# Kernel tuning notes

Hardware: AMD Instinct MI355X
Metric: run time of the kernel (lower is better)

Reference implementation:

```python
import jax, jax.numpy as jnp
import numpy as np

EPS = 1e-8
TINY = 1e-12
C_L1 = float(np.sqrt(3.0 / (4.0 * np.pi)))  # integral-normalized l=1 SH coefficient


def _elu_feature_map(x):
    # positive_feature_map(kind='elu'): elu(x) + 1 > 0
    return jax.nn.elu(x) + 1.0


def _sph_bessel_j1(x):
    # j1(x) = sin(x)/x^2 - cos(x)/x, with series x/3 near 0 for stability
    small = x < 1e-4
    xs = jnp.where(small, 1.0, x)
    return jnp.where(small, x / 3.0, jnp.sin(xs) / (xs * xs) - jnp.cos(xs) / xs)


def setup_inputs() -> dict:
    key = jax.random.key(0)
    k1, k2, k3, k4, k5 = jax.random.split(key, 5)
    B, N, H, D, C, Q = 1, 2048, 8, 32, 32, 8
    pos = jax.random.normal(k1, (B, N, 3), dtype=jnp.float32) * 5.0
    q = jax.random.normal(k2, (B, N, H, D), dtype=jnp.float32)
    k = jax.random.normal(k3, (B, N, H, D), dtype=jnp.float32)
    v = jax.random.normal(k4, (B, N, H, C), dtype=jnp.float32)
    kappa = jnp.linspace(0.5, 4.0, Q, dtype=jnp.float32)          # (Q,) buffer
    a = jax.random.normal(k5, (H, Q), dtype=jnp.float32) * 0.1    # (H,Q) -> 'head' mode
    node_mask = jnp.ones((B, N), dtype=bool)
    return {"pos": pos, "q": q, "k": k, "v": v, "kappa": kappa, "a": a, "node_mask": node_mask}


def reference(pos, q, k, v, kappa, a, node_mask):
    B, N = pos.shape[0], pos.shape[1]
    m = node_mask.astype(pos.dtype)  # (B,N)

    # Linear (kernel) attention: alpha[b,h,i,j] = <phi(q_i), phi(k_j)> / sum_n <phi(q_i), phi(k_n)>
    phi_q = _elu_feature_map(q) * m[:, :, None, None]
    phi_k = _elu_feature_map(k) * m[:, :, None, None]
    v_m = v * m[:, :, None, None]
    logits = jnp.einsum('bihd,bjhd->bhij', phi_q, phi_k)
    denom = jnp.maximum(logits.sum(axis=-1, keepdims=True), EPS)
    alpha = logits / denom  # (B,H,N,N)

    # Pairwise geometry
    r_ij = pos[:, :, None, :] - pos[:, None, :, :]            # (B,N,N,3)
    dist = jnp.sqrt(jnp.sum(r_ij * r_ij, axis=-1) + TINY)     # (B,N,N)
    eye = jnp.eye(N, dtype=bool)
    safe_vec = jnp.array([1.0, 0.0, 0.0], dtype=pos.dtype)
    r_safe = jnp.where(eye[None, :, :, None], safe_vec, r_ij)

    # Real spherical harmonics, l=1, integral normalization, on normalized r_ij
    rn = jnp.sqrt(jnp.sum(r_safe * r_safe, axis=-1, keepdims=True) + TINY)
    Y = C_L1 * (r_safe / rn)  # (B,N,N,3) -> M=3 components

    # Radial part: f[b,h,i,j] = sum_q a[h,q] * j1(dist_ij * kappa_q)
    x = dist[..., None] * kappa  # (B,N,N,Q)
    jl = _sph_bessel_j1(x)
    f = jnp.einsum('bijq,hq->bhij', jl, a)

    # out[b,i,h,m,c] = sum_j alpha*f * Y * v
    w = alpha * f
    out = jnp.einsum('bhij,bijm,bjhc->bihmc', w, Y, v_m)
    return out  # (B, N, H, 2l+1=3, C)
```

## Files before the change

### kernel.cpp

```cpp
#include <hip/hip_runtime.h>

#define NN   2048
#define NH   8
#define ND   32
#define NC   32
#define NQ   8
#define JS   8
#define NOUT (NN*NH*3*NC)
#define EPSV 1e-8f
#define TINYV 1e-12f
#define C_L1 0.4886025119029199f
#define PSCALE 128.0f

typedef _Float16 half8 __attribute__((ext_vector_type(8)));
typedef __fp16   fp16x2 __attribute__((ext_vector_type(2)));
typedef float    f32x4 __attribute__((ext_vector_type(4)));
typedef float    f32x2 __attribute__((ext_vector_type(2)));

__device__ __forceinline__ float phi_elu(float x) { return x > 0.f ? x + 1.f : __expf(x); }
__device__ __forceinline__ float rfl(float x) {
    return __int_as_float(__builtin_amdgcn_readfirstlane(__float_as_int(x)));
}
__device__ __forceinline__ void glds16(const void* g, void* l) {
    __builtin_amdgcn_global_load_lds(
        (const __attribute__((address_space(1))) void*)g,
        (__attribute__((address_space(3))) void*)l, 16, 0, 0);
}

__global__ void k_prep(const float* __restrict__ pos, const float* __restrict__ q,
                       const float* __restrict__ k, const float* __restrict__ v,
                       const float* __restrict__ kappa, const float* __restrict__ a,
                       _Float16* __restrict__ phiQ16, _Float16* __restrict__ KtF,
                       _Float16* __restrict__ VtF, float* __restrict__ posT,
                       float* __restrict__ ksum, float* __restrict__ coef) {
    int b = blockIdx.x, t = threadIdx.x;
    if (b < 256) {
        int h = t >> 5, d = t & 31;
        int dg = d >> 3, e = d & 7;
        float ks = 0.f;
        for (int jj = 0; jj < 8; ++jj) {
            int j = b * 8 + jj;
            float pq = phi_elu(q[j * 256 + t]);
            float pk = phi_elu(k[j * 256 + t]);
            phiQ16[j * 256 + t] = (_Float16)pq;
            int jblk = j >> 5, jin = j & 31, jf = jin >> 4, lo = jin & 15;
            KtF[((((h * 64 + jblk) * 2 + jf) * 64) + dg * 16 + lo) * 8 + e] = (_Float16)pk;
            ks += pk;
        }
        atomicAdd(&ksum[t], ks);
    } else if (b < 512) {
        int unit = (b - 256) * 4 + (t >> 6);
        int lane = t & 63;
        int h = unit >> 7, jblk = (unit >> 1) & 63, cf = unit & 1;
        int hgrp = h >> 1, hh = h & 1;
        int c = cf * 16 + (lane & 15);
        int g8 = lane >> 4;
        half8 w0, w1, w2, w3;
        #pragma unroll
        for (int e = 0; e < 8; ++e) {
            int jl = g8 * 4 + (e & 3) + 16 * (e >> 2);
            int j = jblk * 32 + jl;
            float vv = v[(j * NH + h) * NC + c];
            w0[e] = (_Float16)vv;
            w1[e] = (_Float16)(vv * pos[j * 3 + 0]);
            w2[e] = (_Float16)(vv * pos[j * 3 + 1]);
            w3[e] = (_Float16)(vv * pos[j * 3 + 2]);
        }
        size_t fb = ((size_t)(jblk * 4 + hgrp) * 16 + hh * 2 + cf) * 64 + lane;
        ((half8*)VtF)[fb]        = w0;
        ((half8*)VtF)[fb + 256]  = w1;
        ((half8*)VtF)[fb + 512]  = w2;
        ((half8*)VtF)[fb + 768]  = w3;
    } else if (b < 536) {
        int idx = (b - 512) * 256 + t;
        if (idx < 3 * NN) {
            int comp = idx >> 11, j = idx & 2047;
            posT[comp * NN + j] = pos[j * 3 + comp];
        }
    } else {
        if (t < NH) {
            float An[8];
            #pragma unroll
            for (int n = 0; n < 8; ++n) An[n] = a[t * NQ + n];
            float k0 = kappa[0];
            float ik0 = 1.f / k0, ik02 = ik0 * ik0;
            const float Tc[9][9] = {
                {0,0,0,0,0,0,0,0,0},
                {0,1,0,0,0,0,0,0,0},
                {-1,0,2,0,0,0,0,0,0},
                {0,-3,0,4,0,0,0,0,0},
                {1,0,-8,0,8,0,0,0,0},
                {0,5,0,-20,0,16,0,0,0},
                {-1,0,18,0,-48,0,32,0,0},
                {0,-7,0,56,0,-112,0,64,0},
                {1,0,-32,0,160,0,-256,0,128}};
            const float Uc[9][8] = {
                {0,0,0,0,0,0,0,0},
                {1,0,0,0,0,0,0,0},
                {0,2,0,0,0,0,0,0},
                {-1,0,4,0,0,0,0,0},
                {0,-4,0,8,0,0,0,0},
                {1,0,-12,0,16,0,0,0},
                {0,6,0,-32,0,32,0,0},
                {-1,0,24,0,-80,0,64,0},
                {0,-8,0,80,0,-192,0,128}};
            #pragma unroll
            for (int kk = 0; kk < 9; ++kk) {
                float s = 0.f;
                #pragma unroll
                for (int n = 1; n <= 8; ++n) s = fmaf(An[n-1] * (1.f / n), Tc[n][kk], s);
                coef[kk * 8 + t] = s * ik0;
            }
            #pragma unroll
            for (int kk = 0; kk < 8; ++kk) {
                float s = 0.f;
                #pragma unroll
                for (int n = 1; n <= 8; ++n) s = fmaf(An[n-1] * (1.f / (n * n)), Uc[n][kk], s);
                coef[(9 + kk) * 8 + t] = s * ik02;
            }
        }
    }
}

__global__ __launch_bounds__(256, 3)
void k_main(const float* __restrict__ posT, const _Float16* __restrict__ phiQ16,
            const _Float16* __restrict__ KtF, const _Float16* __restrict__ VtF,
            const float* __restrict__ kappa, const float* __restrict__ coef,
            const float* __restrict__ ksum, _Float16* __restrict__ part) {
    __shared__ __align__(16) char smem[2 * 16384];
    int tid = threadIdx.x;
    int wid = tid >> 6, lane = tid & 63;
    int li = lane & 15, g = lane >> 4;

    int bid = blockIdx.x;
    int hgrp = bid & 3, js = (bid >> 2) & 7, ib = bid >> 5;
    int itile = ib * 64 + wid * 16;

    float k0 = rfl(kappa[0]);

    float pc0[2];
    f32x2 cpq[2][8];
    #pragma unroll
    for (int hh = 0; hh < 2; ++hh) {
        int h = hgrp * 2 + hh;
        pc0[hh] = rfl(coef[h]);
        cpq[hh][0][0] = rfl(coef[8 * 8 + h]);
        cpq[hh][0][1] = rfl(coef[(9 + 7) * 8 + h]);
        #pragma unroll
        for (int kk = 1; kk <= 7; ++kk) {
            cpq[hh][kk][0] = rfl(coef[kk * 8 + h]);
            cpq[hh][kk][1] = rfl(coef[(9 + kk - 1) * 8 + h]);
        }
    }

    half8 qa[2];
    #pragma unroll
    for (int hh = 0; hh < 2; ++hh)
        qa[hh] = ((const half8*)phiQ16)[((size_t)(itile + li) * NH + hgrp * 2 + hh) * 4 + g];

    float pi0 = posT[itile + li];
    float pi1 = posT[NN + itile + li];
    float pi2 = posT[2 * NN + itile + li];

    f32x4 acc[2][4][2];
    #pragma unroll
    for (int hh = 0; hh < 2; ++hh)
      #pragma unroll
      for (int pl = 0; pl < 4; ++pl)
        #pragma unroll
        for (int cf = 0; cf < 2; ++cf)
          acc[hh][pl][cf] = (f32x4){0.f, 0.f, 0.f, 0.f};

    const int j0 = js * (NN / JS);
    const int NCHUNK = (NN / JS) / 32;
    const f32x4 z4 = (f32x4){0.f, 0.f, 0.f, 0.f};
    const int soff = wid * 4096 + lane * 16;

    half8 kf[2][2], kfn[2][2];
    {
        int jblk0 = j0 >> 5;
        #pragma unroll
        for (int hh = 0; hh < 2; ++hh)
            #pragma unroll
            for (int jF = 0; jF < 2; ++jF)
                kf[hh][jF] = ((const half8*)KtF)[
                    (((hgrp * 2 + hh) * 64 + jblk0) * 2 + jF) * 64 + lane];
        size_t sl = (size_t)(jblk0 * 4 + hgrp);
        const char* src = (const char*)VtF + (sl << 14) + soff;
        char* dstl = smem + soff;
        #pragma unroll
        for (int kk = 0; kk < 4; ++kk)
            glds16(src + kk * 1024, dstl + kk * 1024);
    }

    #pragma unroll 1
    for (int t = 0; t < NCHUNK; ++t) {
        int jc = j0 + t * 32, jblk = jc >> 5;

        union { half8 h; fp16x2 p[4]; } wa[2];

        #pragma unroll
        for (int jF = 0; jF < 2; ++jF) {
            f32x4 pj4[3];
            #pragma unroll
            for (int m = 0; m < 3; ++m)
                pj4[m] = *(const f32x4*)(posT + m * NN + jc + jF * 16 + g * 4);

            f32x4 s[2];
            #pragma unroll
            for (int hh = 0; hh < 2; ++hh)
                s[hh] = __builtin_amdgcn_mfma_f32_16x16x32_f16(kf[hh][jF], qa[hh], z4, 0, 0, 0);

            float gux[2][4];
            #pragma unroll
            for (int r = 0; r < 4; ++r) {
                float dx = pi0 - pj4[0][r];
                float dy = pi1 - pj4[1][r];
                float dz = pi2 - pj4[2][r];
                float d2 = fmaf(dx, dx, fmaf(dy, dy, fmaf(dz, dz, TINYV)));
                float u = rsqrtf(d2);
                u = (d2 < 1e-10f) ? 0.f : u;
                float dist = d2 * u;
                float th = dist * k0;
                float sth, cth;
                __sincosf(th, &sth, &cth);
                float e1 = u * u;
                float ws = u * sth;
                f32x2 cc; cc[0] = cth; cc[1] = cth;
                #pragma unroll
                for (int hh = 0; hh < 2; ++hh) {
                    f32x2 pq = cpq[hh][0];
                    #pragma unroll
                    for (int kk = 7; kk >= 1; --kk)
                        pq = __builtin_elementwise_fma(pq, cc, cpq[hh][kk]);
                    float P = fmaf(pq[0], cth, pc0[hh]);
                    float inner = fmaf(ws, pq[1], -P);
                    gux[hh][r] = (s[hh][r] * e1) * inner;
                }
            }
            #pragma unroll
            for (int hh = 0; hh < 2; ++hh) {
                wa[hh].p[jF * 2 + 0] = __builtin_amdgcn_cvt_pkrtz(gux[hh][0], gux[hh][1]);
                wa[hh].p[jF * 2 + 1] = __builtin_amdgcn_cvt_pkrtz(gux[hh][2], gux[hh][3]);
            }
        }

        __syncthreads();

        if (t + 1 < NCHUNK) {
            int jn = jblk + 1;
            #pragma unroll
            for (int hh = 0; hh < 2; ++hh)
                #pragma unroll
                for (int jF = 0; jF < 2; ++jF)
                    kfn[hh][jF] = ((const half8*)KtF)[
                        (((hgrp * 2 + hh) * 64 + jn) * 2 + jF) * 64 + lane];
            size_t sl = (size_t)(jn * 4 + hgrp);
            const char* src = (const char*)VtF + (sl << 14) + soff;
            char* dstl = smem + ((t + 1) & 1) * 16384 + soff;
            #pragma unroll
            for (int kk = 0; kk < 4; ++kk)
                glds16(src + kk * 1024, dstl + kk * 1024);
        }

        const char* vb = smem + (t & 1) * 16384;
        #pragma unroll
        for (int hh = 0; hh < 2; ++hh) {
            #pragma unroll
            for (int pl = 0; pl < 4; ++pl) {
                half8 vf0 = *(const half8*)(vb + ((pl * 4 + hh * 2 + 0) * 1024) + lane * 16);
                half8 vf1 = *(const half8*)(vb + ((pl * 4 + hh * 2 + 1) * 1024) + lane * 16);
                acc[hh][pl][0] = __builtin_amdgcn_mfma_f32_16x16x32_f16(wa[hh].h, vf0, acc[hh][pl][0], 0, 0, 0);
                acc[hh][pl][1] = __builtin_amdgcn_mfma_f32_16x16x32_f16(wa[hh].h, vf1, acc[hh][pl][1], 0, 0, 0);
            }
        }

        if (t + 1 < NCHUNK) {
            #pragma unroll
            for (int hh = 0; hh < 2; ++hh)
                #pragma unroll
                for (int jF = 0; jF < 2; ++jF)
                    kf[hh][jF] = kfn[hh][jF];
        }
    }

    f32x4 pi_ep[3];
    #pragma unroll
    for (int m = 0; m < 3; ++m)
        pi_ep[m] = *(const f32x4*)(posT + m * NN + itile + g * 4);

    float dinvC[2][4];
    #pragma unroll
    for (int hh = 0; hh < 2; ++hh) {
        int h = hgrp * 2 + hh;
        float p = 0.f;
        #pragma unroll
        for (int e = 0; e < 8; ++e) p += (float)qa[hh][e] * ksum[h * 32 + g * 8 + e];
        p += __shfl_xor(p, 16);
        p += __shfl_xor(p, 32);
        float dcol = (C_L1 * PSCALE) / fmaxf(p, EPSV);
        #pragma unroll
        for (int r = 0; r < 4; ++r)
            dinvC[hh][r] = __shfl(dcol, g * 4 + r);
    }

    _Float16* pdst = part + (size_t)js * NOUT;
    #pragma unroll
    for (int hh = 0; hh < 2; ++hh) {
        int h = hgrp * 2 + hh;
        #pragma unroll
        for (int m = 0; m < 3; ++m)
        #pragma unroll
        for (int cf = 0; cf < 2; ++cf)
        #pragma unroll
        for (int r = 0; r < 4; ++r) {
            int i = itile + g * 4 + r;
            size_t idx = ((size_t)i * NH + h) * 96 + m * 32 + cf * 16 + li;
            float val = fmaf(pi_ep[m][r], acc[hh][0][cf][r], -acc[hh][m + 1][cf][r]);
            pdst[idx] = (_Float16)(val * dinvC[hh][r]);
        }
    }
}

__global__ void k_reduce(const _Float16* __restrict__ part, float4* __restrict__ out) {
    int e = blockIdx.x * 256 + threadIdx.x;
    const int NO8 = NOUT / 8;
    if (e >= NO8) return;
    float s[8] = {0.f, 0.f, 0.f, 0.f, 0.f, 0.f, 0.f, 0.f};
    #pragma unroll
    for (int p = 0; p < JS; ++p) {
        half8 t = ((const half8*)part)[(size_t)p * NO8 + e];
        #pragma unroll
        for (int x = 0; x < 8; ++x) s[x] += (float)t[x];
    }
    const float S = 1.f / PSCALE;
    out[e * 2]     = make_float4(s[0] * S, s[1] * S, s[2] * S, s[3] * S);
    out[e * 2 + 1] = make_float4(s[4] * S, s[5] * S, s[6] * S, s[7] * S);
}

extern "C" void kernel_launch(void* const* d_in, const int* in_sizes, int n_in,
                              void* d_out, int out_size, void* d_ws, size_t ws_size,
                              hipStream_t stream) {
    const float* pos   = (const float*)d_in[0];
    const float* q     = (const float*)d_in[1];
    const float* k     = (const float*)d_in[2];
    const float* v     = (const float*)d_in[3];
    const float* kappa = (const float*)d_in[4];
    const float* a     = (const float*)d_in[5];
    float* out = (float*)d_out;
    char* ws = (char*)d_ws;

    _Float16* phiQ16 = (_Float16*)(ws + 0);
    _Float16* KtF    = (_Float16*)(ws + (1u << 20));
    _Float16* VtF    = (_Float16*)(ws + (2u << 20));
    float*    posT   = (float*)   (ws + (6u << 20));
    float*    ksum   = (float*)   (ws + (6u << 20) + 24576);
    float*    coefb  = (float*)   (ws + (6u << 20) + 91136);
    _Float16* partb  = (_Float16*)(ws + (6u << 20) + 131072);

    (void)hipMemsetAsync(ksum, 0, 256 * sizeof(float), stream);
    k_prep<<<537, 256, 0, stream>>>(pos, q, k, v, kappa, a,
                                    phiQ16, KtF, VtF, posT, ksum, coefb);
    k_main<<<(NN / 64) * 4 * JS, 256, 0, stream>>>(posT, phiQ16, KtF, VtF,
                                                   kappa, coefb, ksum, partb);
    k_reduce<<<(NOUT / 8 + 255) / 256, 256, 0, stream>>>(partb, (float4*)out);
}
```

Measured before the change: 68.74 us.

## Stage K and V layout transforms through LDS in prep and drop K register prefetch

The prep kernel now handles whole 32-row blocks per workgroup. It stages phi(k) and v/pos in shared memory, so the transposed KtF and VtF writes become coalesced 16-byte stores instead of scattered halfword writes, and it issues far fewer ksum atomics. The coefficient computation moves into its own tiny kernel, which adds one more launch. In the main kernel, the K fragments are now loaded directly inside the loop instead of being prefetched into registers, and the V LDS prefetch is issued after the MFMA block. This lowers register pressure but exposes K load latency and shortens the window in which the V prefetch can overlap.

```diff
diff --git a/kernel.cpp b/kernel.cpp
--- a/kernel.cpp
+++ b/kernel.cpp
@@ -27,98 +27,113 @@
         (__attribute__((address_space(3))) void*)l, 16, 0, 0);
 }
 
-__global__ void k_prep(const float* __restrict__ pos, const float* __restrict__ q,
-                       const float* __restrict__ k, const float* __restrict__ v,
-                       const float* __restrict__ kappa, const float* __restrict__ a,
-                       _Float16* __restrict__ phiQ16, _Float16* __restrict__ KtF,
-                       _Float16* __restrict__ VtF, float* __restrict__ posT,
-                       float* __restrict__ ksum, float* __restrict__ coef) {
+__global__ __launch_bounds__(256)
+void k_prep(const float* __restrict__ pos, const float* __restrict__ q,
+            const float* __restrict__ k, const float* __restrict__ v,
+            _Float16* __restrict__ phiQ16, _Float16* __restrict__ KtF,
+            _Float16* __restrict__ VtF, float* __restrict__ posT,
+            float* __restrict__ ksum) {
+    __shared__ __align__(16) char smem[33280];
     int b = blockIdx.x, t = threadIdx.x;
-    if (b < 256) {
-        int h = t >> 5, d = t & 31;
-        int dg = d >> 3, e = d & 7;
-        float ks = 0.f;
-        for (int jj = 0; jj < 8; ++jj) {
-            int j = b * 8 + jj;
+    int wid = t >> 6, lane = t & 63;
+    if (b < 64) {
+        _Float16* lds_k = (_Float16*)smem;
+        int jblk = b;
+        #pragma unroll 4
+        for (int jj = 0; jj < 32; ++jj) {
+            int j = jblk * 32 + jj;
             float pq = phi_elu(q[j * 256 + t]);
             float pk = phi_elu(k[j * 256 + t]);
             phiQ16[j * 256 + t] = (_Float16)pq;
-            int jblk = j >> 5, jin = j & 31, jf = jin >> 4, lo = jin & 15;
-            KtF[((((h * 64 + jblk) * 2 + jf) * 64) + dg * 16 + lo) * 8 + e] = (_Float16)pk;
-            ks += pk;
-        }
-        atomicAdd(&ksum[t], ks);
-    } else if (b < 512) {
-        int unit = (b - 256) * 4 + (t >> 6);
-        int lane = t & 63;
-        int h = unit >> 7, jblk = (unit >> 1) & 63, cf = unit & 1;
-        int hgrp = h >> 1, hh = h & 1;
-        int c = cf * 16 + (lane & 15);
-        int g8 = lane >> 4;
-        half8 w0, w1, w2, w3;
-        #pragma unroll
-        for (int e = 0; e < 8; ++e) {
-            int jl = g8 * 4 + (e & 3) + 16 * (e >> 2);
-            int j = jblk * 32 + jl;
-            float vv = v[(j * NH + h) * NC + c];
-            w0[e] = (_Float16)vv;
-            w1[e] = (_Float16)(vv * pos[j * 3 + 0]);
-            w2[e] = (_Float16)(vv * pos[j * 3 + 1]);
-            w3[e] = (_Float16)(vv * pos[j * 3 + 2]);
-        }
-        size_t fb = ((size_t)(jblk * 4 + hgrp) * 16 + hh * 2 + cf) * 64 + lane;
-        ((half8*)VtF)[fb]        = w0;
-        ((half8*)VtF)[fb + 256]  = w1;
-        ((half8*)VtF)[fb + 512]  = w2;
-        ((half8*)VtF)[fb + 768]  = w3;
-    } else if (b < 536) {
-        int idx = (b - 512) * 256 + t;
-        if (idx < 3 * NN) {
-            int comp = idx >> 11, j = idx & 2047;
-            posT[comp * NN + j] = pos[j * 3 + comp];
+            lds_k[jj * 264 + t] = (_Float16)pk;
+        }
+        __syncthreads();
+        float s = 0.f;
+        #pragma unroll
+        for (int jj = 0; jj < 32; ++jj) s += (float)lds_k[jj * 264 + t];
+        atomicAdd(&ksum[t], s);
+        int lo = lane & 15, dg = lane >> 4;
+        #pragma unroll
+        for (int uu = 0; uu < 4; ++uu) {
+            int unit = wid * 4 + uu;
+            int h = unit >> 1, jf = unit & 1;
+            half8 kf = *(const half8*)&lds_k[(jf * 16 + lo) * 264 + h * 32 + dg * 8];
+            ((half8*)KtF)[(size_t)((h * 64 + jblk) * 2 + jf) * 64 + lane] = kf;
         }
     } else {
-        if (t < NH) {
-            float An[8];
-            #pragma unroll
-            for (int n = 0; n < 8; ++n) An[n] = a[t * NQ + n];
-            float k0 = kappa[0];
-            float ik0 = 1.f / k0, ik02 = ik0 * ik0;
-            const float Tc[9][9] = {
-                {0,0,0,0,0,0,0,0,0},
-                {0,1,0,0,0,0,0,0,0},
-                {-1,0,2,0,0,0,0,0,0},
-                {0,-3,0,4,0,0,0,0,0},
-                {1,0,-8,0,8,0,0,0,0},
-                {0,5,0,-20,0,16,0,0,0},
-                {-1,0,18,0,-48,0,32,0,0},
-                {0,-7,0,56,0,-112,0,64,0},
-                {1,0,-32,0,160,0,-256,0,128}};
-            const float Uc[9][8] = {
-                {0,0,0,0,0,0,0,0},
-                {1,0,0,0,0,0,0,0},
-                {0,2,0,0,0,0,0,0},
-                {-1,0,4,0,0,0,0,0},
-                {0,-4,0,8,0,0,0,0},
-                {1,0,-12,0,16,0,0,0},
-                {0,6,0,-32,0,32,0,0},
-                {-1,0,24,0,-80,0,64,0},
-                {0,-8,0,80,0,-192,0,128}};
-            #pragma unroll
-            for (int kk = 0; kk < 9; ++kk) {
-                float s = 0.f;
-                #pragma unroll
-                for (int n = 1; n <= 8; ++n) s = fmaf(An[n-1] * (1.f / n), Tc[n][kk], s);
-                coef[kk * 8 + t] = s * ik0;
-            }
-            #pragma unroll
-            for (int kk = 0; kk < 8; ++kk) {
-                float s = 0.f;
-                #pragma unroll
-                for (int n = 1; n <= 8; ++n) s = fmaf(An[n-1] * (1.f / (n * n)), Uc[n][kk], s);
-                coef[(9 + kk) * 8 + t] = s * ik02;
-            }
-        }
+        float* lds_v = (float*)smem;
+        float* lds_p = (float*)(smem + 32768);
+        int jblk = b - 64;
+        #pragma unroll 4
+        for (int jj = 0; jj < 32; ++jj)
+            lds_v[jj * 256 + t] = v[(size_t)(jblk * 32 + jj) * 256 + t];
+        if (t < 96) lds_p[t] = pos[jblk * 96 + t];
+        __syncthreads();
+        if (t < 96) {
+            int m = t >> 5, jj = t & 31;
+            posT[m * NN + jblk * 32 + jj] = lds_p[jj * 3 + m];
+        }
+        int li = lane & 15, g8 = lane >> 4;
+        #pragma unroll
+        for (int uu = 0; uu < 16; ++uu) {
+            int unit = wid * 16 + uu;
+            int hgrp = unit >> 4, pl = (unit >> 2) & 3, hh = (unit >> 1) & 1, cf = unit & 1;
+            int h = hgrp * 2 + hh, c = cf * 16 + li;
+            half8 w;
+            #pragma unroll
+            for (int e = 0; e < 8; ++e) {
+                int jl = g8 * 4 + (e & 3) + 16 * (e >> 2);
+                float vv = lds_v[jl * 256 + h * 32 + c];
+                float fac = (pl == 0) ? 1.f : lds_p[jl * 3 + (pl - 1)];
+                w[e] = (_Float16)(vv * fac);
+            }
+            ((half8*)VtF)[((size_t)(jblk * 4 + hgrp) * 16 + pl * 4 + hh * 2 + cf) * 64 + lane] = w;
+        }
+    }
+}
+
+__global__ void k_coef(const float* __restrict__ kappa, const float* __restrict__ a,
+                       float* __restrict__ coef) {
+    int t = threadIdx.x;
+    if (t >= NH) return;
+    float An[8];
+    #pragma unroll
+    for (int n = 0; n < 8; ++n) An[n] = a[t * NQ + n];
+    float k0 = kappa[0];
+    float ik0 = 1.f / k0, ik02 = ik0 * ik0;
+    const float Tc[9][9] = {
+        {0,0,0,0,0,0,0,0,0},
+        {0,1,0,0,0,0,0,0,0},
+        {-1,0,2,0,0,0,0,0,0},
+        {0,-3,0,4,0,0,0,0,0},
+        {1,0,-8,0,8,0,0,0,0},
+        {0,5,0,-20,0,16,0,0,0},
+        {-1,0,18,0,-48,0,32,0,0},
+        {0,-7,0,56,0,-112,0,64,0},
+        {1,0,-32,0,160,0,-256,0,128}};
+    const float Uc[9][8] = {
+        {0,0,0,0,0,0,0,0},
+        {1,0,0,0,0,0,0,0},
+        {0,2,0,0,0,0,0,0},
+        {-1,0,4,0,0,0,0,0},
+        {0,-4,0,8,0,0,0,0},
+        {1,0,-12,0,16,0,0,0},
+        {0,6,0,-32,0,32,0,0},
+        {-1,0,24,0,-80,0,64,0},
+        {0,-8,0,80,0,-192,0,128}};
+    #pragma unroll
+    for (int kk = 0; kk < 9; ++kk) {
+        float s = 0.f;
+        #pragma unroll
+        for (int n = 1; n <= 8; ++n) s = fmaf(An[n-1] * (1.f / n), Tc[n][kk], s);
+        coef[kk * 8 + t] = s * ik0;
+    }
+    #pragma unroll
+    for (int kk = 0; kk < 8; ++kk) {
+        float s = 0.f;
+        #pragma unroll
+        for (int n = 1; n <= 8; ++n) s = fmaf(An[n-1] * (1.f / (n * n)), Uc[n][kk], s);
+        coef[(9 + kk) * 8 + t] = s * ik02;
     }
 }
 
@@ -176,16 +191,8 @@
     const f32x4 z4 = (f32x4){0.f, 0.f, 0.f, 0.f};
     const int soff = wid * 4096 + lane * 16;
 
-    half8 kf[2][2], kfn[2][2];
     {
-        int jblk0 = j0 >> 5;
-        #pragma unroll
-        for (int hh = 0; hh < 2; ++hh)
-            #pragma unroll
-            for (int jF = 0; jF < 2; ++jF)
-                kf[hh][jF] = ((const half8*)KtF)[
-                    (((hgrp * 2 + hh) * 64 + jblk0) * 2 + jF) * 64 + lane];
-        size_t sl = (size_t)(jblk0 * 4 + hgrp);
+        size_t sl = (size_t)((j0 >> 5) * 4 + hgrp);
         const char* src = (const char*)VtF + (sl << 14) + soff;
         char* dstl = smem + soff;
         #pragma unroll
@@ -208,8 +215,11 @@
 
             f32x4 s[2];
             #pragma unroll
-            for (int hh = 0; hh < 2; ++hh)
-                s[hh] = __builtin_amdgcn_mfma_f32_16x16x32_f16(kf[hh][jF], qa[hh], z4, 0, 0, 0);
+            for (int hh = 0; hh < 2; ++hh) {
+                int h = hgrp * 2 + hh;
+                half8 kf = ((const half8*)KtF)[(size_t)((h * 64 + jblk) * 2 + jF) * 64 + lane];
+                s[hh] = __builtin_amdgcn_mfma_f32_16x16x32_f16(kf, qa[hh], z4, 0, 0, 0);
+            }
 
             float gux[2][4];
             #pragma unroll
@@ -247,22 +257,6 @@
 
         __syncthreads();
 
-        if (t + 1 < NCHUNK) {
-            int jn = jblk + 1;
-            #pragma unroll
-            for (int hh = 0; hh < 2; ++hh)
-                #pragma unroll
-                for (int jF = 0; jF < 2; ++jF)
-                    kfn[hh][jF] = ((const half8*)KtF)[
-                        (((hgrp * 2 + hh) * 64 + jn) * 2 + jF) * 64 + lane];
-            size_t sl = (size_t)(jn * 4 + hgrp);
-            const char* src = (const char*)VtF + (sl << 14) + soff;
-            char* dstl = smem + ((t + 1) & 1) * 16384 + soff;
-            #pragma unroll
-            for (int kk = 0; kk < 4; ++kk)
-                glds16(src + kk * 1024, dstl + kk * 1024);
-        }
-
         const char* vb = smem + (t & 1) * 16384;
         #pragma unroll
         for (int hh = 0; hh < 2; ++hh) {
@@ -276,11 +270,12 @@
         }
 
         if (t + 1 < NCHUNK) {
-            #pragma unroll
-            for (int hh = 0; hh < 2; ++hh)
-                #pragma unroll
-                for (int jF = 0; jF < 2; ++jF)
-                    kf[hh][jF] = kfn[hh][jF];
+            size_t sl = (size_t)((jblk + 1) * 4 + hgrp);
+            const char* src = (const char*)VtF + (sl << 14) + soff;
+            char* dstl = smem + ((t + 1) & 1) * 16384 + soff;
+            #pragma unroll
+            for (int kk = 0; kk < 4; ++kk)
+                glds16(src + kk * 1024, dstl + kk * 1024);
         }
     }
 
@@ -359,8 +354,8 @@
     _Float16* partb  = (_Float16*)(ws + (6u << 20) + 131072);
 
     (void)hipMemsetAsync(ksum, 0, 256 * sizeof(float), stream);
-    k_prep<<<537, 256, 0, stream>>>(pos, q, k, v, kappa, a,
-                                    phiQ16, KtF, VtF, posT, ksum, coefb);
+    k_prep<<<128, 256, 0, stream>>>(pos, q, k, v, phiQ16, KtF, VtF, posT, ksum);
+    k_coef<<<1, 64, 0, stream>>>(kappa, a, coefb);
     k_main<<<(NN / 64) * 4 * JS, 256, 0, stream>>>(posT, phiQ16, KtF, VtF,
                                                    kappa, coefb, ksum, partb);
     k_reduce<<<(NOUT / 8 + 255) / 256, 256, 0, stream>>>(partb, (float4*)out);
```

After: 65.99 us. -4.0%, faster.
